# Performance work log

Measured on AMD Instinct MI355X. Metric: run time of the kernel, lower is better.

The kernel has to match this reference:

```python
import jax, jax.numpy as jnp
import numpy as np

HEADS = 12
D_HEAD = 64  # d_model // heads


def _split_heads(t, heads, d_head):
    # Faithful to the torch code: transpose(1,2) -> (B, C, T), then
    # reshape (B, -1, heads, d_head), then transpose(1,2) -> (B, heads, T', d_head).
    B = t.shape[0]
    t = jnp.swapaxes(t, 1, 2)                      # (B, C, T)
    t = t.reshape(B, -1, heads, d_head)            # (B, T', heads, d_head) -- layout quirk preserved
    return jnp.swapaxes(t, 1, 2)                   # (B, heads, T', d_head)


def setup_inputs() -> dict:
    key = jax.random.key(0)
    ks = jax.random.split(key, 10)
    B, Tq, Tkv, D = 8, 4096, 77, 768
    s = 0.02
    return {
        "x": jax.random.normal(ks[0], (B, Tq, D), jnp.float32),
        "prompt": jax.random.normal(ks[1], (B, Tkv, D), jnp.float32),
        "Wq": jax.random.normal(ks[2], (D, D), jnp.float32) * s,
        "bq": jax.random.normal(ks[3], (D,), jnp.float32) * s,
        "Wk": jax.random.normal(ks[4], (D, D), jnp.float32) * s,
        "bk": jax.random.normal(ks[5], (D,), jnp.float32) * s,
        "Wv": jax.random.normal(ks[6], (D, D), jnp.float32) * s,
        "bv": jax.random.normal(ks[7], (D,), jnp.float32) * s,
        "Wp": jax.random.normal(ks[8], (D, D), jnp.float32) * s,
        "bp": jax.random.normal(ks[9], (D,), jnp.float32) * s,
    }


def reference(x, prompt, Wq, bq, Wk, bk, Wv, bv, Wp, bp):
    B, Tq, C = x.shape
    Ckv = prompt.shape[-1]
    q = _split_heads(x @ Wq.T + bq, HEADS, D_HEAD)       # (B, H, Tq, d_head)
    k = _split_heads(prompt @ Wk.T + bk, HEADS, D_HEAD)  # (B, H, Tkv, d_head)
    v = _split_heads(prompt @ Wv.T + bv, HEADS, D_HEAD)
    scale = 1.0 / jnp.sqrt(jnp.asarray(Ckv, x.dtype))    # note: sqrt(d_prompt), as in source
    att = jnp.einsum('bhqd,bhkd->bhqk', q, k) * scale
    att = jax.nn.softmax(att, axis=-1)
    out = jnp.einsum('bhqk,bhkd->bhqd', att, v)          # (B, H, Tq, d_head)
    out = jnp.swapaxes(out, 1, 2).reshape(B, Tq, C)
    return out @ Wp.T + bp                               # dropout = identity (eval)
```

## Files before the change

kernel.cpp:

```cpp
#include <hip/hip_runtime.h>

typedef __attribute__((ext_vector_type(8))) __bf16 bf16x8;
typedef __attribute__((ext_vector_type(4))) float f32x4;
typedef __attribute__((ext_vector_type(8))) unsigned short u16x8;
typedef __attribute__((ext_vector_type(4))) unsigned short u16x4;

#define DEV __device__ __forceinline__

DEV float bf2f(unsigned short u) {
  unsigned int x = ((unsigned int)u) << 16;
  return __builtin_bit_cast(float, x);
}
DEV unsigned short f2bf(float f) {
  unsigned int u = __builtin_bit_cast(unsigned int, f);
  u = u + 0x7fffu + ((u >> 16) & 1u);
  return (unsigned short)(u >> 16);
}
DEV unsigned int cvtpk(float a, float b) {
  unsigned int r;
  asm("v_cvt_pk_bf16_f32 %0, %1, %2" : "=v"(r) : "v"(a), "v"(b));
  return r;
}

DEV void glds16(const void* g, void* l) {
  __builtin_amdgcn_global_load_lds(
      (__attribute__((address_space(1))) void*)g,
      (__attribute__((address_space(3))) void*)l, 16, 0, 0);
}

__global__ __launch_bounds__(256) void k_prep(
    const float* __restrict__ x, const float* __restrict__ Wq,
    const float* __restrict__ Wk, const float* __restrict__ Wv,
    const float* __restrict__ Wp, const float* __restrict__ prompt,
    const float* __restrict__ bk, const float* __restrict__ bv,
    unsigned short* __restrict__ xb, unsigned short* __restrict__ wqb,
    unsigned short* __restrict__ wkvb, unsigned short* __restrict__ wpb,
    unsigned short* __restrict__ pb, float* __restrict__ bkv,
    unsigned short* __restrict__ vt2) {
  const int blk = blockIdx.x;
  const int tid = threadIdx.x;
  if (blk < 2048) {
    for (int i = blk * 256 + tid; i < 6291456; i += 524288) {
      float4 v = reinterpret_cast<const float4*>(x)[i];
      u16x4 o;
      o[0] = f2bf(v.x); o[1] = f2bf(v.y); o[2] = f2bf(v.z); o[3] = f2bf(v.w);
      reinterpret_cast<u16x4*>(xb)[i] = o;
    }
  } else if (blk < 4352) {
    const int w = (blk - 2048) / 576;
    const int i = (blk - 2048 - w * 576) * 256 + tid;
    const float* src = (w == 0) ? Wq : (w == 1) ? Wk : (w == 2) ? Wv : Wp;
    unsigned short* dst =
        (w == 0) ? wqb : (w == 1) ? wkvb : (w == 2) ? (wkvb + 589824) : wpb;
    float4 v = reinterpret_cast<const float4*>(src)[i];
    u16x4 o;
    o[0] = f2bf(v.x); o[1] = f2bf(v.y); o[2] = f2bf(v.z); o[3] = f2bf(v.w);
    reinterpret_cast<u16x4*>(dst)[i] = o;
  } else if (blk < 5120) {
    const int i4 = (blk - 4352) * 256 + tid;
    const int e = i4 * 4;
    const int b = e / 98304;
    const int rem = e - b * 98304;
    const int s = rem / 768;
    const int d = rem - s * 768;
    u16x4 o;
    if (s < 77) {
      float4 v = *reinterpret_cast<const float4*>(&prompt[((long)b * 77 + s) * 768 + d]);
      o[0] = f2bf(v.x); o[1] = f2bf(v.y); o[2] = f2bf(v.z); o[3] = f2bf(v.w);
    } else {
      o[0] = 0; o[1] = 0; o[2] = 0; o[3] = 0;
    }
    reinterpret_cast<u16x4*>(pb)[i4] = o;
  } else if (blk < 5126) {
    const int i = (blk - 5120) * 256 + tid;
    if (i < 1536) bkv[i] = (i < 768) ? bk[i] : bv[i - 768];
  } else {
    const int i = (blk - 5126) * 256 + tid;
    u16x8 z = {};
    reinterpret_cast<u16x8*>(vt2)[i] = z;
  }
}

__global__ __launch_bounds__(256, 2) void k_qkv(
    const unsigned short* __restrict__ WQ, const unsigned short* __restrict__ XB,
    unsigned short* __restrict__ QT, const float* __restrict__ BQ,
    const unsigned short* __restrict__ WKV, const unsigned short* __restrict__ PB,
    unsigned short* __restrict__ KV, unsigned short* __restrict__ VT2,
    const float* __restrict__ BKV) {
  __shared__ alignas(16) unsigned short S[17408];
  unsigned short* const As = S;
  unsigned short* const Bs = S + 8192;

  const int tid = threadIdx.x;
  const int wave = tid >> 6;
  const int lane = tid & 63;
  const int wm = (wave >> 1) * 64;
  const int wn = (wave & 1) * 64;
  const int fr = lane & 15;
  const int fk = (lane >> 4) * 8;
  const int srow = lane >> 3;
  const int r0 = (lane >> 4) * 4;

  if (blockIdx.x < 96) {
    const int idx = blockIdx.x;
    const int bz = idx / 12;
    const int tm = (idx - bz * 12) * 128;
    const unsigned short* Bb = PB + (long)bz * 98304;
    const int scol = (lane & 7) * 8;

    f32x4 acc[4][4] = {};
    for (int k0 = 0; k0 < 768; k0 += 64) {
      __syncthreads();
#pragma unroll
      for (int i = 0; i < 4; ++i) {
        const int chunk = i * 4 + wave;
        glds16(WKV + (long)(tm + chunk * 8 + srow) * 768 + (k0 + scol), &As[chunk * 512]);
      }
#pragma unroll
      for (int i = 0; i < 4; ++i) {
        const int chunk = i * 4 + wave;
        glds16(Bb + (long)(chunk * 8 + srow) * 768 + (k0 + scol), &Bs[chunk * 512]);
      }
      __syncthreads();
#pragma unroll
      for (int ks = 0; ks < 2; ++ks) {
        bf16x8 af[4], bf[4];
#pragma unroll
        for (int mi = 0; mi < 4; ++mi)
          af[mi] = *reinterpret_cast<const bf16x8*>(&As[(wm + mi * 16 + fr) * 64 + ks * 32 + fk]);
#pragma unroll
        for (int ni = 0; ni < 4; ++ni)
          bf[ni] = *reinterpret_cast<const bf16x8*>(&Bs[(wn + ni * 16 + fr) * 64 + ks * 32 + fk]);
#pragma unroll
        for (int mi = 0; mi < 4; ++mi)
#pragma unroll
          for (int ni = 0; ni < 4; ++ni)
            acc[mi][ni] =
                __builtin_amdgcn_mfma_f32_16x16x32_bf16(af[mi], bf[ni], acc[mi][ni], 0, 0, 0);
      }
    }
#pragma unroll
    for (int mi = 0; mi < 4; ++mi) {
#pragma unroll
      for (int ni = 0; ni < 4; ++ni) {
        const int col = wn + ni * 16 + fr;
        if (col < 77) {
#pragma unroll
          for (int r = 0; r < 4; ++r) {
            const int row = tm + wm + mi * 16 + r0 + r;
            const unsigned short v = f2bf(acc[mi][ni][r] + BKV[row]);
            if (tm < 768) {
              KV[(long)bz * 59136 + (long)row * 77 + col] = v;
            } else {
              const int p = (row - 768) * 77 + col;
              const int snew = p / 768;
              const int c0 = p - snew * 768;
              VT2[(long)bz * 79872 + (long)c0 * 104 + snew] = v;
            }
          }
        }
      }
    }
    return;
  }

  const int bid = blockIdx.x - 96;
  const int l = (bid & 7) * 192 + (bid >> 3);
  const int tm = (l % 6) * 128;
  const int tn = (l / 6) * 128;
  const int srcx = ((lane & 7) ^ srow) * 8;
  const int rx = (fr & 7) * 8;

  f32x4 acc[4][4] = {};
  for (int k0 = 0; k0 < 768; k0 += 64) {
    __syncthreads();
#pragma unroll
    for (int i = 0; i < 4; ++i) {
      const int chunk = i * 4 + wave;
      glds16(WQ + (long)(tm + chunk * 8 + srow) * 768 + (k0 + srcx), &As[chunk * 512]);
    }
#pragma unroll
    for (int i = 0; i < 4; ++i) {
      const int chunk = i * 4 + wave;
      glds16(XB + (long)(tn + chunk * 8 + srow) * 768 + (k0 + srcx), &Bs[chunk * 512]);
    }
    __syncthreads();
#pragma unroll
    for (int ks = 0; ks < 2; ++ks) {
      bf16x8 af[4], bf[4];
#pragma unroll
      for (int mi = 0; mi < 4; ++mi)
        af[mi] = *reinterpret_cast<const bf16x8*>(
            &As[(wm + mi * 16 + fr) * 64 + ((ks * 32 + fk) ^ rx)]);
#pragma unroll
      for (int ni = 0; ni < 4; ++ni)
        bf[ni] = *reinterpret_cast<const bf16x8*>(
            &Bs[(wn + ni * 16 + fr) * 64 + ((ks * 32 + fk) ^ rx)]);
#pragma unroll
      for (int mi = 0; mi < 4; ++mi)
#pragma unroll
        for (int ni = 0; ni < 4; ++ni)
          acc[mi][ni] =
              __builtin_amdgcn_mfma_f32_16x16x32_bf16(af[mi], bf[ni], acc[mi][ni], 0, 0, 0);
    }
  }

  __syncthreads();
#pragma unroll
  for (int mi = 0; mi < 4; ++mi) {
    const int cmb = wm + mi * 16 + r0;
#pragma unroll
    for (int ni = 0; ni < 4; ++ni) {
      const int ct = wn + ni * 16 + fr;
      const unsigned int p01 =
          cvtpk(acc[mi][ni][0] + BQ[tm + cmb], acc[mi][ni][1] + BQ[tm + cmb + 1]);
      const unsigned int p23 =
          cvtpk(acc[mi][ni][2] + BQ[tm + cmb + 2], acc[mi][ni][3] + BQ[tm + cmb + 3]);
      S[(cmb + 0) * 136 + ct] = (unsigned short)p01;
      S[(cmb + 1) * 136 + ct] = (unsigned short)(p01 >> 16);
      S[(cmb + 2) * 136 + ct] = (unsigned short)p23;
      S[(cmb + 3) * 136 + ct] = (unsigned short)(p23 >> 16);
    }
  }
  __syncthreads();
  const int b_ = tn >> 12;
  const int toff = tn & 4095;
  const int cm = tid >> 1;
  const int t8 = (tid & 1) * 64;
  const long gb = (long)b_ * 3145728 + (long)(tm + cm) * 4096 + toff + t8;
#pragma unroll
  for (int j = 0; j < 8; ++j)
    *reinterpret_cast<u16x8*>(&QT[gb + j * 8]) =
        *reinterpret_cast<const u16x8*>(&S[cm * 136 + t8 + j * 8]);
}

__global__ __launch_bounds__(256, 2) void k_gout(const unsigned short* __restrict__ A,
                                                 const unsigned short* __restrict__ B,
                                                 float* __restrict__ out,
                                                 const float* __restrict__ bias) {
  __shared__ alignas(16) unsigned short S[16384];
  unsigned short* const As = S;
  unsigned short* const Bs = S + 8192;

  const int tid = threadIdx.x;
  const int wave = tid >> 6;
  const int lane = tid & 63;
  const int l = (blockIdx.x & 7) * 192 + (blockIdx.x >> 3);
  const int tm = (l / 6) * 128;
  const int tn = (l % 6) * 128;
  const int wm = (wave >> 1) * 64;
  const int wn = (wave & 1) * 64;
  const int fr = lane & 15;
  const int fk = (lane >> 4) * 8;
  const int srow = lane >> 3;
  const int srcx = ((lane & 7) ^ srow) * 8;
  const int rx = (fr & 7) * 8;

  f32x4 acc[4][4] = {};

  for (int k0 = 0; k0 < 768; k0 += 64) {
    __syncthreads();
#pragma unroll
    for (int i = 0; i < 4; ++i) {
      const int chunk = i * 4 + wave;
      glds16(A + (long)(tm + chunk * 8 + srow) * 768 + (k0 + srcx), &As[chunk * 512]);
    }
#pragma unroll
    for (int i = 0; i < 4; ++i) {
      const int chunk = i * 4 + wave;
      glds16(B + (long)(tn + chunk * 8 + srow) * 768 + (k0 + srcx), &Bs[chunk * 512]);
    }
    __syncthreads();
#pragma unroll
    for (int ks = 0; ks < 2; ++ks) {
      bf16x8 af[4], bf[4];
#pragma unroll
      for (int mi = 0; mi < 4; ++mi)
        af[mi] = *reinterpret_cast<const bf16x8*>(
            &As[(wm + mi * 16 + fr) * 64 + ((ks * 32 + fk) ^ rx)]);
#pragma unroll
      for (int ni = 0; ni < 4; ++ni)
        bf[ni] = *reinterpret_cast<const bf16x8*>(
            &Bs[(wn + ni * 16 + fr) * 64 + ((ks * 32 + fk) ^ rx)]);
#pragma unroll
      for (int mi = 0; mi < 4; ++mi)
#pragma unroll
        for (int ni = 0; ni < 4; ++ni)
          acc[mi][ni] =
              __builtin_amdgcn_mfma_f32_16x16x32_bf16(af[mi], bf[ni], acc[mi][ni], 0, 0, 0);
    }
  }

  const int r0 = (lane >> 4) * 4;
#pragma unroll
  for (int mi = 0; mi < 4; ++mi) {
#pragma unroll
    for (int ni = 0; ni < 4; ++ni) {
      const int col = tn + wn + ni * 16 + fr;
      const float bv = bias[col];
#pragma unroll
      for (int r = 0; r < 4; ++r) {
        const long g = tm + wm + mi * 16 + r0 + r;
        out[g * 768 + col] = acc[mi][ni][r] + bv;
      }
    }
  }
}

__global__ __launch_bounds__(256, 4) void k_attn(const unsigned short* __restrict__ QT,
                                                 const unsigned short* __restrict__ KVT,
                                                 const unsigned short* __restrict__ VT2,
                                                 unsigned short* __restrict__ Y) {
  __shared__ alignas(16) unsigned short Plds[128 * 104];
  __shared__ alignas(16) unsigned short Vt[64 * 104];

  const int b = blockIdx.z;
  const int h = blockIdx.y;
  const int tid = threadIdx.x;
  const int wave = tid >> 6;
  const int lane = tid & 63;
  const int fr = lane & 15;
  const int fg = lane >> 4;

  const unsigned short* vsrc = VT2 + (long)b * 79872 + h * 6656;
#pragma unroll
  for (int r = 0; r < 4; ++r) {
    const int chunk = r * 256 + tid;
    if (chunk < 832) glds16(vsrc + chunk * 8, &Vt[chunk * 8]);
  }

  {
    const int row = wave * 32 + (lane >> 1);
    u16x8 z = {};
    *reinterpret_cast<u16x8*>(&Plds[row * 104 + 80 + (lane & 1) * 8]) = z;
  }

  const int t0 = blockIdx.x * 128 + wave * 32;
  const long qb = (long)b * 3145728 + h * 64;
  const long kflat = (long)b * 59136 + h * 64;

  bf16x8 qa[2][2];
#pragma unroll
  for (int m = 0; m < 2; ++m)
#pragma unroll
    for (int ks = 0; ks < 2; ++ks)
      qa[m][ks] = *reinterpret_cast<const bf16x8*>(
          &QT[qb + (long)(t0 + m * 16 + fr) * 768 + ks * 32 + fg * 8]);

  bf16x8 kb[5][2];
#pragma unroll
  for (int n = 0; n < 5; ++n)
#pragma unroll
    for (int ks = 0; ks < 2; ++ks)
      kb[n][ks] = *reinterpret_cast<const bf16x8*>(
          &KVT[kflat + (long)(n * 16 + fr) * 768 + ks * 32 + fg * 8]);

  f32x4 s_[2][5] = {};
#pragma unroll
  for (int ks = 0; ks < 2; ++ks)
#pragma unroll
    for (int m = 0; m < 2; ++m)
#pragma unroll
      for (int n = 0; n < 5; ++n)
        s_[m][n] = __builtin_amdgcn_mfma_f32_16x16x32_bf16(qa[m][ks], kb[n][ks], s_[m][n], 0, 0, 0);

  const float scale = 0.036084391824351615f;
  f32x4 rl[2];
#pragma unroll
  for (int m = 0; m < 2; ++m) {
#pragma unroll
    for (int n = 0; n < 5; ++n) {
      const int key = n * 16 + fr;
#pragma unroll
      for (int r = 0; r < 4; ++r)
        s_[m][n][r] = (key < 77) ? __expf(s_[m][n][r] * scale) : 0.f;
    }
    f32x4 t = s_[m][0] + s_[m][1] + s_[m][2] + s_[m][3] + s_[m][4];
#pragma unroll
    for (int w = 1; w < 16; w <<= 1) {
      f32x4 u;
#pragma unroll
      for (int r = 0; r < 4; ++r) u[r] = __shfl_xor(t[r], w);
      t += u;
    }
    rl[m][0] = 1.f / t[0]; rl[m][1] = 1.f / t[1];
    rl[m][2] = 1.f / t[2]; rl[m][3] = 1.f / t[3];
  }

#pragma unroll
  for (int m = 0; m < 2; ++m)
#pragma unroll
    for (int n = 0; n < 5; ++n) {
      const unsigned int p01 = cvtpk(s_[m][n][0], s_[m][n][1]);
      const unsigned int p23 = cvtpk(s_[m][n][2], s_[m][n][3]);
      const int base = wave * 32 + m * 16 + fg * 4;
      const int col = n * 16 + fr;
      Plds[(base + 0) * 104 + col] = (unsigned short)p01;
      Plds[(base + 1) * 104 + col] = (unsigned short)(p01 >> 16);
      Plds[(base + 2) * 104 + col] = (unsigned short)p23;
      Plds[(base + 3) * 104 + col] = (unsigned short)(p23 >> 16);
    }

  __syncthreads();

  f32x4 o[2][4] = {};
#pragma unroll
  for (int ks = 0; ks < 3; ++ks) {
    bf16x8 pa[2], vb[4];
#pragma unroll
    for (int m = 0; m < 2; ++m)
      pa[m] = *reinterpret_cast<const bf16x8*>(
          &Plds[(wave * 32 + m * 16 + fr) * 104 + ks * 32 + fg * 8]);
#pragma unroll
    for (int n = 0; n < 4; ++n)
      vb[n] = *reinterpret_cast<const bf16x8*>(&Vt[(n * 16 + fr) * 104 + ks * 32 + fg * 8]);
#pragma unroll
    for (int m = 0; m < 2; ++m)
#pragma unroll
      for (int n = 0; n < 4; ++n)
        o[m][n] = __builtin_amdgcn_mfma_f32_16x16x32_bf16(pa[m], vb[n], o[m][n], 0, 0, 0);
  }

#pragma unroll
  for (int m = 0; m < 2; ++m)
#pragma unroll
    for (int n = 0; n < 4; ++n) {
      const unsigned int p01 = cvtpk(o[m][n][0] * rl[m][0], o[m][n][1] * rl[m][1]);
      const unsigned int p23 = cvtpk(o[m][n][2] * rl[m][2], o[m][n][3] * rl[m][3]);
      const int base = wave * 32 + m * 16 + fg * 4;
      const int col = n * 16 + fr;
      Plds[(base + 0) * 104 + col] = (unsigned short)p01;
      Plds[(base + 1) * 104 + col] = (unsigned short)(p01 >> 16);
      Plds[(base + 2) * 104 + col] = (unsigned short)p23;
      Plds[(base + 3) * 104 + col] = (unsigned short)(p23 >> 16);
    }
#pragma unroll
  for (int j = 0; j < 4; ++j) {
    const int chunk = j * 64 + lane;
    const int row = chunk >> 3;
    const int d8 = (chunk & 7) * 8;
    *reinterpret_cast<u16x8*>(&Y[qb + (long)(t0 + row) * 768 + d8]) =
        *reinterpret_cast<const u16x8*>(&Plds[(wave * 32 + row) * 104 + d8]);
  }
}

extern "C" void kernel_launch(void* const* d_in, const int* in_sizes, int n_in,
                              void* d_out, int out_size, void* d_ws, size_t ws_size,
                              hipStream_t stream) {
  const float* x      = (const float*)d_in[0];
  const float* prompt = (const float*)d_in[1];
  const float* Wq     = (const float*)d_in[2];
  const float* bq     = (const float*)d_in[3];
  const float* Wk     = (const float*)d_in[4];
  const float* bk     = (const float*)d_in[5];
  const float* Wv     = (const float*)d_in[6];
  const float* bv     = (const float*)d_in[7];
  const float* Wp     = (const float*)d_in[8];
  const float* bp     = (const float*)d_in[9];
  float* out = (float*)d_out;

  if (ws_size < 109185024u) return;
  char* ws = (char*)d_ws;
  unsigned short* xb   = (unsigned short*)(ws + 0);
  unsigned short* y    = xb;
  unsigned short* qt   = (unsigned short*)(ws + 50331648L);
  unsigned short* wqb  = (unsigned short*)(ws + 100663296L);
  unsigned short* wpb  = (unsigned short*)(ws + 101842944L);
  unsigned short* wkvb = (unsigned short*)(ws + 103022592L);
  unsigned short* pb   = (unsigned short*)(ws + 105381888L);
  unsigned short* kvt  = (unsigned short*)(ws + 106954752L);
  unsigned short* vt2  = (unsigned short*)(ws + 107900928L);
  float*          bkv  = (float*)(ws + 109178880L);

  k_prep<<<5438, 256, 0, stream>>>(x, Wq, Wk, Wv, Wp, prompt, bk, bv,
                                   xb, wqb, wkvb, wpb, pb, bkv, vt2);

  k_qkv<<<1632, 256, 0, stream>>>(wqb, xb, qt, bq, wkvb, pb, kvt, vt2, bkv);

  k_attn<<<dim3(32, 12, 8), 256, 0, stream>>>(qt, kvt, vt2, y);

  k_gout<<<1536, 256, 0, stream>>>(y, wpb, out, bp);
}
```

Baseline: 166.0 us.

## Double K-tile depth in Q and output GEMMs and raise priority around attention MFMAs

The Q-projection and output-projection GEMMs now stage 128-wide K slices in LDS per iteration instead of 64, using a two-half swizzled layout. This halves the number of barrier pairs per tile. LDS use grows to 64 KB per block, which may limit occupancy against the launch bound of 2 blocks per CU. The attention kernel also wraps its MFMA loops in s_setprio raises so waves in the matrix phase get scheduling priority.

```diff
diff --git a/kernel.cpp b/kernel.cpp
--- a/kernel.cpp
+++ b/kernel.cpp
@@ -87,9 +87,7 @@
     const unsigned short* __restrict__ WKV, const unsigned short* __restrict__ PB,
     unsigned short* __restrict__ KV, unsigned short* __restrict__ VT2,
     const float* __restrict__ BKV) {
-  __shared__ alignas(16) unsigned short S[17408];
-  unsigned short* const As = S;
-  unsigned short* const Bs = S + 8192;
+  __shared__ alignas(16) unsigned short S[32768];
 
   const int tid = threadIdx.x;
   const int wave = tid >> 6;
@@ -102,6 +100,8 @@
   const int r0 = (lane >> 4) * 4;
 
   if (blockIdx.x < 96) {
+    unsigned short* const As = S;
+    unsigned short* const Bs = S + 8192;
     const int idx = blockIdx.x;
     const int bz = idx / 12;
     const int tm = (idx - bz * 12) * 128;
@@ -170,32 +170,44 @@
   const int tn = (l / 6) * 128;
   const int srcx = ((lane & 7) ^ srow) * 8;
   const int rx = (fr & 7) * 8;
+  unsigned short* const Aq = S;
+  unsigned short* const Bq = S + 16384;
 
   f32x4 acc[4][4] = {};
-  for (int k0 = 0; k0 < 768; k0 += 64) {
+  for (int k0 = 0; k0 < 768; k0 += 128) {
     __syncthreads();
 #pragma unroll
-    for (int i = 0; i < 4; ++i) {
-      const int chunk = i * 4 + wave;
-      glds16(WQ + (long)(tm + chunk * 8 + srow) * 768 + (k0 + srcx), &As[chunk * 512]);
-    }
-#pragma unroll
-    for (int i = 0; i < 4; ++i) {
-      const int chunk = i * 4 + wave;
-      glds16(XB + (long)(tn + chunk * 8 + srow) * 768 + (k0 + srcx), &Bs[chunk * 512]);
+    for (int i = 0; i < 8; ++i) {
+      const int c = i * 4 + wave;
+      const int u = c >> 1;
+      const int kh = (c & 1) * 64;
+      glds16(WQ + (long)(tm + u * 8 + srow) * 768 + (k0 + kh + srcx), &Aq[c * 512]);
+    }
+#pragma unroll
+    for (int i = 0; i < 8; ++i) {
+      const int c = i * 4 + wave;
+      const int u = c >> 1;
+      const int kh = (c & 1) * 64;
+      glds16(XB + (long)(tn + u * 8 + srow) * 768 + (k0 + kh + srcx), &Bq[c * 512]);
     }
     __syncthreads();
 #pragma unroll
-    for (int ks = 0; ks < 2; ++ks) {
+    for (int ks = 0; ks < 4; ++ks) {
+      const int col = ks * 32 + fk;
+      const int cbase = ((col >> 6) << 9) + ((col & 63) ^ rx);
       bf16x8 af[4], bf[4];
 #pragma unroll
-      for (int mi = 0; mi < 4; ++mi)
+      for (int mi = 0; mi < 4; ++mi) {
+        const int row = wm + mi * 16 + fr;
         af[mi] = *reinterpret_cast<const bf16x8*>(
-            &As[(wm + mi * 16 + fr) * 64 + ((ks * 32 + fk) ^ rx)]);
-#pragma unroll
-      for (int ni = 0; ni < 4; ++ni)
+            &Aq[(row >> 3) * 1024 + (row & 7) * 64 + cbase]);
+      }
+#pragma unroll
+      for (int ni = 0; ni < 4; ++ni) {
+        const int row = wn + ni * 16 + fr;
         bf[ni] = *reinterpret_cast<const bf16x8*>(
-            &Bs[(wn + ni * 16 + fr) * 64 + ((ks * 32 + fk) ^ rx)]);
+            &Bq[(row >> 3) * 1024 + (row & 7) * 64 + cbase]);
+      }
 #pragma unroll
       for (int mi = 0; mi < 4; ++mi)
 #pragma unroll
@@ -238,9 +250,9 @@
                                                  const unsigned short* __restrict__ B,
                                                  float* __restrict__ out,
                                                  const float* __restrict__ bias) {
-  __shared__ alignas(16) unsigned short S[16384];
+  __shared__ alignas(16) unsigned short S[32768];
   unsigned short* const As = S;
-  unsigned short* const Bs = S + 8192;
+  unsigned short* const Bs = S + 16384;
 
   const int tid = threadIdx.x;
   const int wave = tid >> 6;
@@ -258,30 +270,40 @@
 
   f32x4 acc[4][4] = {};
 
-  for (int k0 = 0; k0 < 768; k0 += 64) {
+  for (int k0 = 0; k0 < 768; k0 += 128) {
     __syncthreads();
 #pragma unroll
-    for (int i = 0; i < 4; ++i) {
-      const int chunk = i * 4 + wave;
-      glds16(A + (long)(tm + chunk * 8 + srow) * 768 + (k0 + srcx), &As[chunk * 512]);
-    }
-#pragma unroll
-    for (int i = 0; i < 4; ++i) {
-      const int chunk = i * 4 + wave;
-      glds16(B + (long)(tn + chunk * 8 + srow) * 768 + (k0 + srcx), &Bs[chunk * 512]);
+    for (int i = 0; i < 8; ++i) {
+      const int c = i * 4 + wave;
+      const int u = c >> 1;
+      const int kh = (c & 1) * 64;
+      glds16(A + (long)(tm + u * 8 + srow) * 768 + (k0 + kh + srcx), &As[c * 512]);
+    }
+#pragma unroll
+    for (int i = 0; i < 8; ++i) {
+      const int c = i * 4 + wave;
+      const int u = c >> 1;
+      const int kh = (c & 1) * 64;
+      glds16(B + (long)(tn + u * 8 + srow) * 768 + (k0 + kh + srcx), &Bs[c * 512]);
     }
     __syncthreads();
 #pragma unroll
-    for (int ks = 0; ks < 2; ++ks) {
+    for (int ks = 0; ks < 4; ++ks) {
+      const int col = ks * 32 + fk;
+      const int cbase = ((col >> 6) << 9) + ((col & 63) ^ rx);
       bf16x8 af[4], bf[4];
 #pragma unroll
-      for (int mi = 0; mi < 4; ++mi)
+      for (int mi = 0; mi < 4; ++mi) {
+        const int row = wm + mi * 16 + fr;
         af[mi] = *reinterpret_cast<const bf16x8*>(
-            &As[(wm + mi * 16 + fr) * 64 + ((ks * 32 + fk) ^ rx)]);
-#pragma unroll
-      for (int ni = 0; ni < 4; ++ni)
+            &As[(row >> 3) * 1024 + (row & 7) * 64 + cbase]);
+      }
+#pragma unroll
+      for (int ni = 0; ni < 4; ++ni) {
+        const int row = wn + ni * 16 + fr;
         bf[ni] = *reinterpret_cast<const bf16x8*>(
-            &Bs[(wn + ni * 16 + fr) * 64 + ((ks * 32 + fk) ^ rx)]);
+            &Bs[(row >> 3) * 1024 + (row & 7) * 64 + cbase]);
+      }
 #pragma unroll
       for (int mi = 0; mi < 4; ++mi)
 #pragma unroll
@@ -356,6 +378,7 @@
           &KVT[kflat + (long)(n * 16 + fr) * 768 + ks * 32 + fg * 8]);
 
   f32x4 s_[2][5] = {};
+  __builtin_amdgcn_s_setprio(1);
 #pragma unroll
   for (int ks = 0; ks < 2; ++ks)
 #pragma unroll
@@ -363,6 +386,7 @@
 #pragma unroll
       for (int n = 0; n < 5; ++n)
         s_[m][n] = __builtin_amdgcn_mfma_f32_16x16x32_bf16(qa[m][ks], kb[n][ks], s_[m][n], 0, 0, 0);
+  __builtin_amdgcn_s_setprio(0);
 
   const float scale = 0.036084391824351615f;
   f32x4 rl[2];
@@ -404,6 +428,7 @@
   __syncthreads();
 
   f32x4 o[2][4] = {};
+  __builtin_amdgcn_s_setprio(1);
 #pragma unroll
   for (int ks = 0; ks < 3; ++ks) {
     bf16x8 pa[2], vb[4];
@@ -420,6 +445,7 @@
       for (int n = 0; n < 4; ++n)
         o[m][n] = __builtin_amdgcn_mfma_f32_16x16x32_bf16(pa[m], vb[n], o[m][n], 0, 0, 0);
   }
+  __builtin_amdgcn_s_setprio(0);
 
 #pragma unroll
   for (int m = 0; m < 2; ++m)
```

After: 168.4 us. No clear change (+1.4%).
